# Optimization experiments

Hardware: AMD Instinct MI355X
Metric: run time of the kernel (lower is better)

The kernel has to match this reference:

```python
import jax, jax.numpy as jnp
import numpy as np

N = 50000   # nodes
E = 800000  # edges (avg degree 16)
D = 128     # in_dim == out_dim
EPS = 1e-5  # LayerNorm eps (torch default)


def setup_inputs() -> dict:
    key = jax.random.key(0)
    ks = jax.random.split(key, 8)
    x = jax.random.normal(ks[0], (N, D), dtype=jnp.float32)
    edge_row = jax.random.randint(ks[1], (E,), 0, N, dtype=jnp.int32)
    edge_col = jax.random.randint(ks[2], (E,), 0, N, dtype=jnp.int32)
    edge_val = jax.random.uniform(ks[3], (E,), dtype=jnp.float32)
    W = jax.random.normal(ks[4], (D, D), dtype=jnp.float32) / np.sqrt(D).astype(np.float32)
    b = jnp.zeros((D,), jnp.float32)
    gamma = jnp.ones((D,), jnp.float32)
    beta = jnp.zeros((D,), jnp.float32)
    return {"x": x, "edge_val": edge_val, "W": W, "b": b,
            "gamma": gamma, "beta": beta,
            "edge_row": edge_row, "edge_col": edge_col}


def reference(x, edge_val, W, b, gamma, beta, edge_row, edge_col):
    # SpMM: support = adj @ x, adj in COO form (row, col, val)
    msgs = edge_val[:, None] * x[edge_col]                      # [E, D] gather
    support = jax.ops.segment_sum(msgs, edge_row, num_segments=x.shape[0])  # [N, D]
    # Linear (torch stores weight as [out, in])
    h = support @ W.T + b                                       # [N, D]
    # LayerNorm over last dim
    mu = jnp.mean(h, axis=-1, keepdims=True)
    var = jnp.mean(jnp.square(h - mu), axis=-1, keepdims=True)
    h = (h - mu) * jax.lax.rsqrt(var + EPS) * gamma + beta
    # ReLU; dropout is identity at inference
    return jax.nn.relu(h)
```

## Files before the change

kernel.cpp:

```cpp
#include <hip/hip_runtime.h>

#define D 128
#define LN_EPS 1e-5f
#define RPB 16
#define POISON 0xAAAAAAAAu
#define BINSTRIDE 4864
#define CSRSTRIDE 5632
#define SBF_STRIDE 68

typedef __attribute__((ext_vector_type(8))) short short8;
typedef __attribute__((ext_vector_type(4))) float f32x4;

union FragU { uint4 u; short8 s; };

__device__ __forceinline__ unsigned bf16_hi(float f) {
    unsigned u = __float_as_uint(f);
    return (u + 0x7FFFu + ((u >> 16) & 1u)) & 0xFFFF0000u;
}
__device__ __forceinline__ float lo16f(unsigned u) { return __uint_as_float(u << 16); }
__device__ __forceinline__ float hi16f(unsigned u) { return __uint_as_float(u & 0xFFFF0000u); }

__global__ void __launch_bounds__(256) conv_kernel(
    const float* __restrict__ x, unsigned* __restrict__ xb16,
    const float* __restrict__ W, unsigned* __restrict__ Wb,
    int n8, int half) {
    int gid = blockIdx.x * 256 + threadIdx.x;
    if (gid < 8192) {
        int u  = gid & 3;
        int L  = (gid >> 2) & 63;
        int nt = (gid >> 8) & 7;
        int kt = gid >> 11;
        int n = nt * 16 + (L & 15);
        int k = kt * 32 + (L >> 4) * 8 + u * 2;
        unsigned lo = bf16_hi(W[n * D + k]) >> 16;
        unsigned hi = bf16_hi(W[n * D + k + 1]);
        Wb[gid] = hi | lo;
    }
#pragma unroll
    for (int kk = 0; kk < 2; ++kk) {
        int j = gid + kk * half;
        if (j < n8) {
            float4 a = *(const float4*)(x + (size_t)j * 8);
            float4 c = *(const float4*)(x + (size_t)j * 8 + 4);
            uint4 o;
            o.x = bf16_hi(a.y) | (bf16_hi(a.x) >> 16);
            o.y = bf16_hi(a.w) | (bf16_hi(a.z) >> 16);
            o.z = bf16_hi(c.y) | (bf16_hi(c.x) >> 16);
            o.w = bf16_hi(c.w) | (bf16_hi(c.z) >> 16);
            *(uint4*)(xb16 + (size_t)j * 4) = o;
        }
    }
}

__global__ void __launch_bounds__(256) pass1_kernel(
    const int* __restrict__ edge_row, const int* __restrict__ edge_col,
    const float* __restrict__ edge_val,
    unsigned* __restrict__ bin_cursor, uint2* __restrict__ binbuf,
    int E, int nbins, int epb) {
    __shared__ int cntL[256];
    __shared__ int curL[256];
    __shared__ int baseL[256];
    int t = threadIdx.x;
    cntL[t] = 0;
    __syncthreads();
    int e0 = blockIdx.x * epb;
    int e1 = e0 + epb; if (e1 > E) e1 = E;
    for (int i = e0 + t; i < e1; i += 256)
        atomicAdd(&cntL[edge_row[i] >> 8], 1);
    __syncthreads();
    if (t < nbins) {
        int c = cntL[t];
        baseL[t] = c ? (int)(atomicAdd(&bin_cursor[t], (unsigned)c) - POISON) : 0;
    }
    curL[t] = 0;
    __syncthreads();
    for (int i = e0 + t; i < e1; i += 256) {
        int r = edge_row[i];
        int bin = r >> 8;
        int p = atomicAdd(&curL[bin], 1) + baseL[bin];
        if (p < BINSTRIDE) {
            uint2 rec;
            rec.x = ((unsigned)edge_col[i] << 16) | (unsigned)(r & 255);
            rec.y = bf16_hi(edge_val[i]);
            binbuf[(size_t)bin * BINSTRIDE + p] = rec;
        }
    }
}

__global__ void __launch_bounds__(256) pass2_kernel(
    const uint2* __restrict__ binbuf, const unsigned* __restrict__ bin_cursor,
    unsigned* __restrict__ csr, int* __restrict__ offsets,
    int* __restrict__ degs, int N, int nbins) {
    __shared__ int tmp[2][256];
    __shared__ int rcnt[256];
    __shared__ int rcur[256];
    __shared__ int roff[256];
    int t = threadIdx.x;
    int b = blockIdx.x;

    int sz = (int)(bin_cursor[b] - POISON);
    if (sz > BINSTRIDE) sz = BINSTRIDE;
    if (sz < 0) sz = 0;
    rcnt[t] = 0;
    __syncthreads();

    const uint2* bb = binbuf + (size_t)b * BINSTRIDE;
    int base = b * CSRSTRIDE;

    for (int i = t; i < sz; i += 256)
        atomicAdd(&rcnt[bb[i].x & 255], 1);
    __syncthreads();

    int rpad = (rcnt[t] + 3) & ~3;
    tmp[0][t] = rpad;
    __syncthreads();
    int buf = 0;
    for (int off = 1; off < 256; off <<= 1) {
        int xv = tmp[buf][t];
        if (t >= off) xv += tmp[buf][t - off];
        tmp[1 - buf][t] = xv;
        buf ^= 1;
        __syncthreads();
    }
    roff[t] = tmp[buf][t] - rpad;
    rcur[t] = 0;
    int row = (b << 8) + t;
    if (row < N) {
        offsets[row] = base + roff[t];
        degs[row] = rpad;
    }
    __syncthreads();

    for (int i = t; i < sz; i += 256) {
        uint2 rec = bb[i];
        int rl = rec.x & 255;
        int p = atomicAdd(&rcur[rl], 1);
        csr[base + roff[rl] + p] = rec.y | (rec.x >> 16);
    }
    __syncthreads();

    int c0 = rcnt[t];
    for (int k = c0; k < rpad; ++k)
        csr[base + roff[t] + k] = 0;
}

__global__ void __launch_bounds__(256) fused_gather_linear(
    const unsigned* __restrict__ xb16, const unsigned* __restrict__ csr,
    const int* __restrict__ offsets, const int* __restrict__ degs,
    const unsigned* __restrict__ Wb, const float* __restrict__ b,
    const float* __restrict__ gamma, const float* __restrict__ beta,
    float* __restrict__ out, int N) {
    __shared__ unsigned sbf[RPB][SBF_STRIDE];
    __shared__ float sh[RPB][D];
    __shared__ float mu_s[RPB], inv_s[RPB];
    int t = threadIdx.x;
    int row0 = blockIdx.x * RPB;

    {
        int r = t >> 4;
        int q = t & 15;
        int row = row0 + r;
        float4 accA = make_float4(0.f, 0.f, 0.f, 0.f);
        float4 accB = make_float4(0.f, 0.f, 0.f, 0.f);
        if (row < N) {
            const unsigned* ce = csr + offsets[row];
            int pd = degs[row];
            const unsigned* xb = xb16 + q * 4;
            for (int e = 0; e < pd; e += 4) {
                uint4 p = *(const uint4*)(ce + e);
                unsigned c0 = p.x & 0xFFFFu, c1 = p.y & 0xFFFFu;
                unsigned c2 = p.z & 0xFFFFu, c3 = p.w & 0xFFFFu;
                float w0 = __uint_as_float(p.x & 0xFFFF0000u);
                float w1 = __uint_as_float(p.y & 0xFFFF0000u);
                float w2 = __uint_as_float(p.z & 0xFFFF0000u);
                float w3 = __uint_as_float(p.w & 0xFFFF0000u);
                uint4 X0 = *(const uint4*)(xb + (size_t)c0 * (D / 2));
                uint4 X1 = *(const uint4*)(xb + (size_t)c1 * (D / 2));
                uint4 X2 = *(const uint4*)(xb + (size_t)c2 * (D / 2));
                uint4 X3 = *(const uint4*)(xb + (size_t)c3 * (D / 2));
                accA.x = fmaf(w0, lo16f(X0.x), accA.x);
                accA.y = fmaf(w0, hi16f(X0.x), accA.y);
                accA.z = fmaf(w0, lo16f(X0.y), accA.z);
                accA.w = fmaf(w0, hi16f(X0.y), accA.w);
                accB.x = fmaf(w0, lo16f(X0.z), accB.x);
                accB.y = fmaf(w0, hi16f(X0.z), accB.y);
                accB.z = fmaf(w0, lo16f(X0.w), accB.z);
                accB.w = fmaf(w0, hi16f(X0.w), accB.w);
                accA.x = fmaf(w1, lo16f(X1.x), accA.x);
                accA.y = fmaf(w1, hi16f(X1.x), accA.y);
                accA.z = fmaf(w1, lo16f(X1.y), accA.z);
                accA.w = fmaf(w1, hi16f(X1.y), accA.w);
                accB.x = fmaf(w1, lo16f(X1.z), accB.x);
                accB.y = fmaf(w1, hi16f(X1.z), accB.y);
                accB.z = fmaf(w1, lo16f(X1.w), accB.z);
                accB.w = fmaf(w1, hi16f(X1.w), accB.w);
                accA.x = fmaf(w2, lo16f(X2.x), accA.x);
                accA.y = fmaf(w2, hi16f(X2.x), accA.y);
                accA.z = fmaf(w2, lo16f(X2.y), accA.z);
                accA.w = fmaf(w2, hi16f(X2.y), accA.w);
                accB.x = fmaf(w2, lo16f(X2.z), accB.x);
                accB.y = fmaf(w2, hi16f(X2.z), accB.y);
                accB.z = fmaf(w2, lo16f(X2.w), accB.z);
                accB.w = fmaf(w2, hi16f(X2.w), accB.w);
                accA.x = fmaf(w3, lo16f(X3.x), accA.x);
                accA.y = fmaf(w3, hi16f(X3.x), accA.y);
                accA.z = fmaf(w3, lo16f(X3.y), accA.z);
                accA.w = fmaf(w3, hi16f(X3.y), accA.w);
                accB.x = fmaf(w3, lo16f(X3.z), accB.x);
                accB.y = fmaf(w3, hi16f(X3.z), accB.y);
                accB.z = fmaf(w3, lo16f(X3.w), accB.z);
                accB.w = fmaf(w3, hi16f(X3.w), accB.w);
            }
        }
        uint4 o;
        o.x = bf16_hi(accA.y) | (bf16_hi(accA.x) >> 16);
        o.y = bf16_hi(accA.w) | (bf16_hi(accA.z) >> 16);
        o.z = bf16_hi(accB.y) | (bf16_hi(accB.x) >> 16);
        o.w = bf16_hi(accB.w) | (bf16_hi(accB.z) >> 16);
        *(uint4*)&sbf[r][q * 4] = o;
    }
    __syncthreads();

    {
        int L = t & 63;
        int w = t >> 6;
        int m = L & 15;
        int g = L >> 4;
        f32x4 acc0 = {0.f, 0.f, 0.f, 0.f};
        f32x4 acc1 = {0.f, 0.f, 0.f, 0.f};
#pragma unroll
        for (int kt = 0; kt < 4; ++kt) {
            FragU a, b0, b1;
            a.u  = *(const uint4*)&sbf[m][kt * 16 + g * 4];
            b0.u = *(const uint4*)(Wb + (((size_t)(kt * 8 + w * 2)) * 64 + L) * 4);
            b1.u = *(const uint4*)(Wb + (((size_t)(kt * 8 + w * 2 + 1)) * 64 + L) * 4);
            acc0 = __builtin_amdgcn_mfma_f32_16x16x32_bf16(a.s, b0.s, acc0, 0, 0, 0);
            acc1 = __builtin_amdgcn_mfma_f32_16x16x32_bf16(a.s, b1.s, acc1, 0, 0, 0);
        }
        int n0 = w * 32 + m;
        int n1 = n0 + 16;
        float bv0 = b[n0], bv1 = b[n1];
#pragma unroll
        for (int i = 0; i < 4; ++i) {
            int rr = g * 4 + i;
            sh[rr][n0] = acc0[i] + bv0;
            sh[rr][n1] = acc1[i] + bv1;
        }
    }
    __syncthreads();

    {
        int rr = t >> 4, j = t & 15;
        float sum = 0.f, sq = 0.f;
#pragma unroll
        for (int i = 0; i < 8; ++i) {
            float v = sh[rr][j + 16 * i];
            sum += v;
            sq = fmaf(v, v, sq);
        }
#pragma unroll
        for (int off = 8; off > 0; off >>= 1) {
            sum += __shfl_down(sum, off, 16);
            sq  += __shfl_down(sq, off, 16);
        }
        if (j == 0) {
            float mu = sum * (1.0f / D);
            float var = sq * (1.0f / D) - mu * mu;
            mu_s[rr] = mu;
            inv_s[rr] = rsqrtf(var + LN_EPS);
        }
    }
    __syncthreads();

    {
        int td = t & 127;
        int rbase = (t >> 7) * 8;
        float g = gamma[td], be = beta[td];
#pragma unroll
        for (int r = 0; r < 8; ++r) {
            int row = row0 + rbase + r;
            if (row < N) {
                float y = (sh[rbase + r][td] - mu_s[rbase + r]) * inv_s[rbase + r] * g + be;
                out[(size_t)row * D + td] = fmaxf(y, 0.f);
            }
        }
    }
}

extern "C" void kernel_launch(void* const* d_in, const int* in_sizes, int n_in,
                              void* d_out, int out_size, void* d_ws, size_t ws_size,
                              hipStream_t stream) {
    const float* x        = (const float*)d_in[0];
    const float* edge_val = (const float*)d_in[1];
    const float* W        = (const float*)d_in[2];
    const float* b        = (const float*)d_in[3];
    const float* gamma    = (const float*)d_in[4];
    const float* beta     = (const float*)d_in[5];
    const int*   edge_row = (const int*)d_in[6];
    const int*   edge_col = (const int*)d_in[7];

    const int N = in_sizes[0] / D;
    const int E = in_sizes[1];
    const int n8 = N * D / 8;
    const int nbins = (N + 255) >> 8;

    char* ws = (char*)d_ws;
    uint2*    binbuf     = (uint2*)ws;     ws += (size_t)nbins * BINSTRIDE * sizeof(uint2);
    unsigned* xb16       = (unsigned*)ws;  ws += (size_t)N * (D / 2) * sizeof(unsigned);
    unsigned* csr        = (unsigned*)ws;  ws += (size_t)nbins * CSRSTRIDE * sizeof(unsigned);
    unsigned* Wb         = (unsigned*)ws;  ws += 8192 * sizeof(unsigned);
    int*      offsets    = (int*)ws;       ws += (size_t)N * sizeof(int);
    int*      degs       = (int*)ws;       ws += (size_t)N * sizeof(int);
    unsigned* bin_cursor = (unsigned*)ws;  ws += 256 * sizeof(unsigned);

    {
        int half = (n8 + 1) / 2;
        int blocks = (half + 255) / 256;
        conv_kernel<<<blocks, 256, 0, stream>>>(x, xb16, W, Wb, n8, half);
    }
    {
        int epb = (E + 255) / 256;
        pass1_kernel<<<256, 256, 0, stream>>>(edge_row, edge_col, edge_val,
                                              bin_cursor, binbuf, E, nbins, epb);
    }
    pass2_kernel<<<nbins, 256, 0, stream>>>(binbuf, bin_cursor, csr, offsets,
                                            degs, N, nbins);
    fused_gather_linear<<<(N + RPB - 1) / RPB, 256, 0, stream>>>(
        xb16, csr, offsets, degs, Wb, b, gamma, beta, (float*)d_out, N);
}
```

Baseline: 155.0 us.

## Fuse bf16 conversion into edge binning kernel with vectorized edge loads

Merges the x/W bf16 conversion kernel and the first edge-binning pass into one kernel launched with 512 blocks, using a grid-stride loop for the x conversion. Edge row/col/val are now read as int4/float4 vectors, four edges per thread, for both the count and scatter phases. The aim is to drop one kernel launch and to use memory bandwidth better across more blocks. The trade-off is that each block must finish its conversion work before it starts binning, and the record order inside bins changes.

```diff
diff --git a/kernel.cpp b/kernel.cpp
--- a/kernel.cpp
+++ b/kernel.cpp
@@ -7,6 +7,7 @@
 #define BINSTRIDE 4864
 #define CSRSTRIDE 5632
 #define SBF_STRIDE 68
+#define P1BLOCKS 512
 
 typedef __attribute__((ext_vector_type(8))) short short8;
 typedef __attribute__((ext_vector_type(4))) float f32x4;
@@ -20,11 +21,22 @@
 __device__ __forceinline__ float lo16f(unsigned u) { return __uint_as_float(u << 16); }
 __device__ __forceinline__ float hi16f(unsigned u) { return __uint_as_float(u & 0xFFFF0000u); }
 
-__global__ void __launch_bounds__(256) conv_kernel(
-    const float* __restrict__ x, unsigned* __restrict__ xb16,
-    const float* __restrict__ W, unsigned* __restrict__ Wb,
-    int n8, int half) {
-    int gid = blockIdx.x * 256 + threadIdx.x;
+__global__ void __launch_bounds__(256) prep1_kernel(
+    const int* __restrict__ edge_row, const int* __restrict__ edge_col,
+    const float* __restrict__ edge_val,
+    const float* __restrict__ W, const float* __restrict__ x,
+    unsigned* __restrict__ Wb, unsigned* __restrict__ xb16,
+    unsigned* __restrict__ bin_cursor, uint2* __restrict__ binbuf,
+    int E, int n8, int nbins, int epb) {
+    __shared__ int cntL[256];
+    __shared__ int curL[256];
+    __shared__ int baseL[256];
+    int t = threadIdx.x;
+    int gid = blockIdx.x * 256 + t;
+    int gsz = gridDim.x * 256;
+
+    cntL[t] = 0;
+
     if (gid < 8192) {
         int u  = gid & 3;
         int L  = (gid >> 2) & 63;
@@ -36,37 +48,33 @@
         unsigned hi = bf16_hi(W[n * D + k + 1]);
         Wb[gid] = hi | lo;
     }
-#pragma unroll
-    for (int kk = 0; kk < 2; ++kk) {
-        int j = gid + kk * half;
-        if (j < n8) {
-            float4 a = *(const float4*)(x + (size_t)j * 8);
-            float4 c = *(const float4*)(x + (size_t)j * 8 + 4);
-            uint4 o;
-            o.x = bf16_hi(a.y) | (bf16_hi(a.x) >> 16);
-            o.y = bf16_hi(a.w) | (bf16_hi(a.z) >> 16);
-            o.z = bf16_hi(c.y) | (bf16_hi(c.x) >> 16);
-            o.w = bf16_hi(c.w) | (bf16_hi(c.z) >> 16);
-            *(uint4*)(xb16 + (size_t)j * 4) = o;
-        }
-    }
-}
-
-__global__ void __launch_bounds__(256) pass1_kernel(
-    const int* __restrict__ edge_row, const int* __restrict__ edge_col,
-    const float* __restrict__ edge_val,
-    unsigned* __restrict__ bin_cursor, uint2* __restrict__ binbuf,
-    int E, int nbins, int epb) {
-    __shared__ int cntL[256];
-    __shared__ int curL[256];
-    __shared__ int baseL[256];
-    int t = threadIdx.x;
-    cntL[t] = 0;
-    __syncthreads();
+
+    for (int j = gid; j < n8; j += gsz) {
+        float4 a = *(const float4*)(x + (size_t)j * 8);
+        float4 c = *(const float4*)(x + (size_t)j * 8 + 4);
+        uint4 o;
+        o.x = bf16_hi(a.y) | (bf16_hi(a.x) >> 16);
+        o.y = bf16_hi(a.w) | (bf16_hi(a.z) >> 16);
+        o.z = bf16_hi(c.y) | (bf16_hi(c.x) >> 16);
+        o.w = bf16_hi(c.w) | (bf16_hi(c.z) >> 16);
+        *(uint4*)(xb16 + (size_t)j * 4) = o;
+    }
+    __syncthreads();
+
     int e0 = blockIdx.x * epb;
     int e1 = e0 + epb; if (e1 > E) e1 = E;
-    for (int i = e0 + t; i < e1; i += 256)
-        atomicAdd(&cntL[edge_row[i] >> 8], 1);
+
+    {
+        int i = e0 + t * 4;
+        for (; i + 3 < e1; i += 1024) {
+            int4 r = *(const int4*)(edge_row + i);
+            atomicAdd(&cntL[r.x >> 8], 1);
+            atomicAdd(&cntL[r.y >> 8], 1);
+            atomicAdd(&cntL[r.z >> 8], 1);
+            atomicAdd(&cntL[r.w >> 8], 1);
+        }
+        for (; i < e1; ++i) atomicAdd(&cntL[edge_row[i] >> 8], 1);
+    }
     __syncthreads();
     if (t < nbins) {
         int c = cntL[t];
@@ -74,15 +82,39 @@
     }
     curL[t] = 0;
     __syncthreads();
-    for (int i = e0 + t; i < e1; i += 256) {
-        int r = edge_row[i];
-        int bin = r >> 8;
-        int p = atomicAdd(&curL[bin], 1) + baseL[bin];
-        if (p < BINSTRIDE) {
-            uint2 rec;
-            rec.x = ((unsigned)edge_col[i] << 16) | (unsigned)(r & 255);
-            rec.y = bf16_hi(edge_val[i]);
-            binbuf[(size_t)bin * BINSTRIDE + p] = rec;
+
+    {
+        int i = e0 + t * 4;
+        for (; i + 3 < e1; i += 1024) {
+            int4 r = *(const int4*)(edge_row + i);
+            int4 c = *(const int4*)(edge_col + i);
+            float4 v = *(const float4*)(edge_val + i);
+            int b0 = r.x >> 8, b1 = r.y >> 8, b2 = r.z >> 8, b3 = r.w >> 8;
+            int p0 = atomicAdd(&curL[b0], 1) + baseL[b0];
+            int p1 = atomicAdd(&curL[b1], 1) + baseL[b1];
+            int p2 = atomicAdd(&curL[b2], 1) + baseL[b2];
+            int p3 = atomicAdd(&curL[b3], 1) + baseL[b3];
+            if (p0 < BINSTRIDE)
+                binbuf[(size_t)b0 * BINSTRIDE + p0] =
+                    make_uint2(((unsigned)c.x << 16) | (unsigned)(r.x & 255), bf16_hi(v.x));
+            if (p1 < BINSTRIDE)
+                binbuf[(size_t)b1 * BINSTRIDE + p1] =
+                    make_uint2(((unsigned)c.y << 16) | (unsigned)(r.y & 255), bf16_hi(v.y));
+            if (p2 < BINSTRIDE)
+                binbuf[(size_t)b2 * BINSTRIDE + p2] =
+                    make_uint2(((unsigned)c.z << 16) | (unsigned)(r.z & 255), bf16_hi(v.z));
+            if (p3 < BINSTRIDE)
+                binbuf[(size_t)b3 * BINSTRIDE + p3] =
+                    make_uint2(((unsigned)c.w << 16) | (unsigned)(r.w & 255), bf16_hi(v.w));
+        }
+        for (; i < e1; ++i) {
+            int r = edge_row[i];
+            int bin = r >> 8;
+            int p = atomicAdd(&curL[bin], 1) + baseL[bin];
+            if (p < BINSTRIDE)
+                binbuf[(size_t)bin * BINSTRIDE + p] =
+                    make_uint2(((unsigned)edge_col[i] << 16) | (unsigned)(r & 255),
+                               bf16_hi(edge_val[i]));
         }
     }
 }
@@ -313,16 +345,11 @@
     int*      degs       = (int*)ws;       ws += (size_t)N * sizeof(int);
     unsigned* bin_cursor = (unsigned*)ws;  ws += 256 * sizeof(unsigned);
 
-    {
-        int half = (n8 + 1) / 2;
-        int blocks = (half + 255) / 256;
-        conv_kernel<<<blocks, 256, 0, stream>>>(x, xb16, W, Wb, n8, half);
-    }
-    {
-        int epb = (E + 255) / 256;
-        pass1_kernel<<<256, 256, 0, stream>>>(edge_row, edge_col, edge_val,
-                                              bin_cursor, binbuf, E, nbins, epb);
-    }
+    int epb = ((E + P1BLOCKS - 1) / P1BLOCKS + 3) & ~3;
+
+    prep1_kernel<<<P1BLOCKS, 256, 0, stream>>>(edge_row, edge_col, edge_val,
+                                               W, x, Wb, xb16, bin_cursor,
+                                               binbuf, E, n8, nbins, epb);
     pass2_kernel<<<nbins, 256, 0, stream>>>(binbuf, bin_cursor, csr, offsets,
                                             degs, N, nbins);
     fused_gather_linear<<<(N + RPB - 1) / RPB, 256, 0, stream>>>(
```

Result: faster. 150.3 us (-3.1%).
